# Performance work log

Measured on AMD Instinct MI355X. Metric: run time of the kernel, lower is better.

## Reference

```python
import jax, jax.numpy as jnp
import numpy as np

H, D = 4, 32  # num_heads, per-head out dim (out_feats=128)
N_AGENT, N_GT, N_UAV = 50000, 50000, 50000
E = 600000
IN = 64


def _gat(x_src, x_dst, src, dst, W_src, W_dst, al, ar, W_res, b, num_dst):
    """DGL-style bipartite GATConv with residual, bias and ReLU activation."""
    fs = (x_src @ W_src).reshape(-1, H, D)      # [Ns,H,D]
    fd = (x_dst @ W_dst).reshape(-1, H, D)      # [Nd,H,D]
    el = jnp.sum(fs * al, axis=-1)              # [Ns,H]
    er = jnp.sum(fd * ar, axis=-1)              # [Nd,H]
    e = jax.nn.leaky_relu(el[src] + er[dst], 0.2)          # [E,H]
    # segment softmax over incoming edges of each dst node
    emax = jax.ops.segment_max(e, dst, num_segments=num_dst)   # [Nd,H], -inf for deg-0
    ee = jnp.exp(e - emax[dst])
    denom = jax.ops.segment_sum(ee, dst, num_segments=num_dst)
    a = ee / denom[dst]                          # [E,H]
    msg = fs[src] * a[:, :, None]                # [E,H,D]
    rst = jax.ops.segment_sum(msg, dst, num_segments=num_dst)  # [Nd,H,D]; zeros for deg-0
    res = (x_dst @ W_res).reshape(-1, H, D)      # residual projection
    out = jax.nn.relu(rst + res + b.reshape(1, H, D))
    return out.reshape(num_dst, H * D)


def setup_inputs() -> dict:
    key = jax.random.key(0)
    ks = jax.random.split(key, 20)
    s = 0.1  # weight init scale
    return {
        'x_gt': jax.random.normal(ks[0], (N_GT, IN), jnp.float32),
        'x_uav': jax.random.normal(ks[1], (N_UAV, IN), jnp.float32),
        'x_agent': jax.random.normal(ks[2], (N_AGENT, IN), jnp.float32),
        'src_gt': jax.random.randint(ks[3], (E,), 0, N_GT, jnp.int32),
        'dst_gt': jax.random.randint(ks[4], (E,), 0, N_AGENT, jnp.int32),
        'src_uav': jax.random.randint(ks[5], (E,), 0, N_UAV, jnp.int32),
        'dst_uav': jax.random.randint(ks[6], (E,), 0, N_AGENT, jnp.int32),
        'W_src_gt': s * jax.random.normal(ks[7], (IN, H * D), jnp.float32),
        'W_dst_gt': s * jax.random.normal(ks[8], (IN, H * D), jnp.float32),
        'attn_l_gt': s * jax.random.normal(ks[9], (H, D), jnp.float32),
        'attn_r_gt': s * jax.random.normal(ks[10], (H, D), jnp.float32),
        'W_res_gt': s * jax.random.normal(ks[11], (IN, H * D), jnp.float32),
        'b_gt': jnp.zeros((H * D,), jnp.float32),
        'W_src_uav': s * jax.random.normal(ks[12], (IN, H * D), jnp.float32),
        'W_dst_uav': s * jax.random.normal(ks[13], (IN, H * D), jnp.float32),
        'attn_l_uav': s * jax.random.normal(ks[14], (H, D), jnp.float32),
        'attn_r_uav': s * jax.random.normal(ks[15], (H, D), jnp.float32),
        'W_res_uav': s * jax.random.normal(ks[16], (IN, H * D), jnp.float32),
        'b_uav': jnp.zeros((H * D,), jnp.float32),
        'W_f': s * jax.random.normal(ks[17], (2 * H * D, H * D), jnp.float32),
        'b_f': jnp.zeros((H * D,), jnp.float32),
    }


def reference(x_gt, x_uav, x_agent, src_gt, dst_gt, src_uav, dst_uav,
              W_src_gt, W_dst_gt, attn_l_gt, attn_r_gt, W_res_gt, b_gt,
              W_src_uav, W_dst_uav, attn_l_uav, attn_r_uav, W_res_uav, b_uav,
              W_f, b_f):
    h_gt = _gat(x_gt, x_agent, src_gt, dst_gt, W_src_gt, W_dst_gt,
                attn_l_gt, attn_r_gt, W_res_gt, b_gt, N_AGENT)
    h_uav = _gat(x_uav, x_agent, src_uav, dst_uav, W_src_uav, W_dst_uav,
                 attn_l_uav, attn_r_uav, W_res_uav, b_uav, N_AGENT)
    h = jnp.concatenate([h_gt, h_uav], axis=1)   # [N_agent, 256]
    return jax.nn.relu(h @ W_f + b_f)            # [N_agent, 128]
```

## Files before the change

### kernel.cpp

```cpp
#include <hip/hip_runtime.h>
#include <hip/hip_bf16.h>

using bf16 = __hip_bfloat16;

#define NA 50000
#define NE 600000

typedef __attribute__((ext_vector_type(8))) short short8;
typedef __attribute__((ext_vector_type(4))) float f32x4;

#define HBUF_B   0u
#define FS_B     25600000u
#define EL_B     51200000u
#define RECS_B   54400000u
#define CNT_B    73600000u
#define ROW_B    74000000u
#define TOPS_B   74400016u
#define FLAG_B   74400528u
#define WST_GT_B 74400544u
#define WST_UAV_B 74416928u
#define WRT_B    74433312u
#define WFT_B    74466080u
#define ELT_GT_B 74531616u
#define ELT_UAV_B 74533664u
#define ERT_B    74535712u
#define RANK_B   74537760u
#define WS_BYTES 79337760u

__device__ __forceinline__ float b2f(bf16 v) { return __bfloat162float(v); }

__device__ __forceinline__ float ldf(const void* p, size_t i, int f32) {
    return f32 ? ((const float*)p)[i] : b2f(((const bf16*)p)[i]);
}

__device__ __forceinline__ unsigned short f2bs(float v) {
    bf16 t = __float2bfloat16(v);
    return *(unsigned short*)&t;
}

__device__ __forceinline__ float lrelu_exp(float v) {
    v = v > 0.f ? v : 0.2f * v;
    return __expf(v);
}

__device__ __forceinline__ unsigned int pack_bf16x2(float a, float b) {
    return (unsigned int)f2bs(a) | ((unsigned int)f2bs(b) << 16);
}

__device__ __forceinline__ float lo_f(unsigned int u) { return __uint_as_float(u << 16); }
__device__ __forceinline__ float hi_f(unsigned int u) { return __uint_as_float(u & 0xffff0000u); }

__device__ __forceinline__ short8 ldfrag8(const void* p, size_t off, int f32) {
    if (!f32) return *(const short8*)((const unsigned short*)p + off);
    union { short8 s; unsigned int u[4]; } r;
    const float* fp = (const float*)p + off;
#pragma unroll
    for (int j = 0; j < 4; ++j) r.u[j] = pack_bf16x2(fp[2 * j], fp[2 * j + 1]);
    return r.s;
}

__device__ int probe_f32(const void* x0) {
    __shared__ int cnt;
    if (threadIdx.x == 0) cnt = 0;
    __syncthreads();
    const bf16* p = (const bf16*)x0;
    int bad = 0;
    for (int i = threadIdx.x; i < 1024; i += 256) {
        float av = fabsf(b2f(p[i]));
        if (!(av <= 1e6f)) bad++;
    }
    if (bad) atomicAdd(&cnt, bad);
    __syncthreads();
    return cnt > 8;
}

__global__ void HeteroVisionConv_29703993819529_kernel(
    const void* x0,
    const void* Wsg, const void* alg, const void* Wdg, const void* arg_,
    const void* Wsu, const void* alu, const void* Wdu, const void* aru,
    const void* Wrg, const void* Wru, const void* Wf,
    const int* dg, const int* du, unsigned int* cnt, unsigned int* rank,
    unsigned short* wsT_gt, unsigned short* wsT_uav, unsigned short* wrT,
    unsigned short* wfT, unsigned short* elT_gt, unsigned short* elT_uav,
    unsigned short* erT,
    int* flag, unsigned int* outp, long sent) {
    int b = blockIdx.x, t = threadIdx.x;
    if (b >= 21) {
        int idx = (b - 21) * 256 + t;
        if (idx >= 300000) return;
        int g = idx >= 150000;
        int e = (idx - g * 150000) * 4;
        int4 d4 = *(const int4*)((g ? du : dg) + e);
        unsigned int* c = cnt + g * NA;
        uint4 r4;
        r4.x = atomicAdd(&c[d4.x], 1u);
        r4.y = atomicAdd(&c[d4.y], 1u);
        r4.z = atomicAdd(&c[d4.z], 1u);
        r4.w = atomicAdd(&c[d4.w], 1u);
        *(uint4*)(rank + (size_t)g * NE + e) = r4;
        return;
    }
    int f32 = probe_f32(x0);
    if (b == 20) {
        if (t == 0) { flag[0] = f32; outp[sent] = 0x447A447Au; }
        return;
    }
    if (b < 8) {
        for (int i = t; i < 16 * 256; i += 256) {
            int n = b * 16 + (i >> 8), k = i & 255;
            wfT[n * 256 + k] = f2bs(ldf(Wf, (size_t)k * 128 + n, f32));
        }
    } else if (b < 12) {
        for (int i = t; i < 64 * 64; i += 256) {
            int n = (b - 8) * 64 + (i >> 6), k = i & 63;
            float v = (n < 128) ? ldf(Wrg, (size_t)k * 128 + n, f32)
                                : ldf(Wru, (size_t)k * 128 + (n - 128), f32);
            wrT[n * 64 + k] = f2bs(v);
        }
    } else if (b < 14) {
        for (int i = t; i < 64 * 64; i += 256) {
            int n = (b - 12) * 64 + (i >> 6), k = i & 63;
            wsT_gt[n * 64 + k] = f2bs(ldf(Wsg, (size_t)k * 128 + n, f32));
        }
    } else if (b < 16) {
        for (int i = t; i < 64 * 64; i += 256) {
            int n = (b - 14) * 64 + (i >> 6), k = i & 63;
            wsT_uav[n * 64 + k] = f2bs(ldf(Wsu, (size_t)k * 128 + n, f32));
        }
    } else {
        int m = b - 16;
        const void* Wm = (m == 0) ? Wsg : (m == 1) ? Wdg : (m == 2) ? Wsu : Wdu;
        const void* Am = (m == 0) ? alg : (m == 1) ? arg_ : (m == 2) ? alu : aru;
        int k = t >> 2, h = t & 3;
        float a = 0.f;
        for (int d = 0; d < 32; ++d)
            a += ldf(Wm, (size_t)k * 128 + h * 32 + d, f32) *
                 ldf(Am, (size_t)h * 32 + d, f32);
        unsigned short v = f2bs(a);
        if (m == 0) {
            elT_gt[h * 64 + k] = v;
            for (int i = t; i < 12 * 64; i += 256) elT_gt[(4 + (i >> 6)) * 64 + (i & 63)] = 0;
        } else if (m == 2) {
            elT_uav[h * 64 + k] = v;
            for (int i = t; i < 12 * 64; i += 256) elT_uav[(4 + (i >> 6)) * 64 + (i & 63)] = 0;
        } else if (m == 1) {
            erT[h * 64 + k] = v;
        } else {
            erT[(4 + h) * 64 + k] = v;
            for (int i = t; i < 8 * 64; i += 256) erT[(8 + (i >> 6)) * 64 + (i & 63)] = 0;
        }
    }
}

__global__ void node_fs_k(const void* xg, const void* xu,
                          const unsigned short* wsT_gt, const unsigned short* wsT_uav,
                          const unsigned short* elT_gt, const unsigned short* elT_uav,
                          float* elbase, bf16* fs, const int* flag) {
    int f32 = *flag;
    int bx = blockIdx.x, g = bx / 782, b = bx % 782;
    const void* A = g ? xu : xg;
    const unsigned short* WT = g ? wsT_uav : wsT_gt;
    const unsigned short* ET = g ? elT_uav : elT_gt;
    float* elout = elbase + (g ? 400000 : 0);
    bf16* out = fs + (size_t)g * NA * 128;
    __shared__ unsigned short Bt[128 * 72];
    int t = threadIdx.x;
    for (int i = t * 8; i < 128 * 64; i += 256 * 8) {
        short8 v = *(const short8*)(WT + i);
        int n = i >> 6, k = i & 63;
        *(short8*)&Bt[n * 72 + k] = v;
    }
    __syncthreads();
    int lane = t & 63, w = t >> 6;
    int m = lane & 15, quad = lane >> 4;
    int row = b * 64 + w * 16 + m;
    int rowc = row < NA ? row : NA - 1;
    short8 a0 = ldfrag8(A, (size_t)rowc * 64 + quad * 8, f32);
    short8 a1 = ldfrag8(A, (size_t)rowc * 64 + 32 + quad * 8, f32);
    f32x4 acc[8];
#pragma unroll
    for (int nt = 0; nt < 8; ++nt) acc[nt] = (f32x4){0.f, 0.f, 0.f, 0.f};
#pragma unroll
    for (int nt = 0; nt < 8; ++nt) {
        short8 b0 = *(const short8*)&Bt[(nt * 16 + m) * 72 + quad * 8];
        short8 b1 = *(const short8*)&Bt[(nt * 16 + m) * 72 + 32 + quad * 8];
        acc[nt] = __builtin_amdgcn_mfma_f32_16x16x32_bf16(a0, b0, acc[nt], 0, 0, 0);
        acc[nt] = __builtin_amdgcn_mfma_f32_16x16x32_bf16(a1, b1, acc[nt], 0, 0, 0);
    }
    f32x4 eacc = (f32x4){0.f, 0.f, 0.f, 0.f};
    {
        short8 e0 = *(const short8*)&ET[m * 64 + quad * 8];
        short8 e1 = *(const short8*)&ET[m * 64 + 32 + quad * 8];
        eacc = __builtin_amdgcn_mfma_f32_16x16x32_bf16(a0, e0, eacc, 0, 0, 0);
        eacc = __builtin_amdgcn_mfma_f32_16x16x32_bf16(a1, e1, eacc, 0, 0, 0);
    }
    int srow = b * 64 + w * 16 + quad * 4;
#pragma unroll
    for (int nt = 0; nt < 8; ++nt) {
#pragma unroll
        for (int r = 0; r < 4; ++r) {
            int rr = srow + r;
            if (rr < NA) out[(size_t)rr * 128 + nt * 16 + m] = __float2bfloat16(acc[nt][r]);
        }
    }
    if (m < 4) {
#pragma unroll
        for (int r = 0; r < 4; ++r) {
            int rr = srow + r;
            if (rr < NA) elout[(size_t)rr * 4 + m] = eacc[r];
        }
    }
}

__global__ void res_k(const void* xa, const unsigned short* wrT,
                      const unsigned short* erT,
                      const void* bg, const void* bu,
                      float* elbase, bf16* hbuf, const int* flag) {
    int f32 = *flag;
    int b = blockIdx.x;
    __shared__ unsigned short Bt[256 * 72];
    __shared__ float bl[256];
    int t = threadIdx.x;
    for (int i = t * 8; i < 256 * 64; i += 256 * 8) {
        short8 v = *(const short8*)(wrT + i);
        int n = i >> 6, k = i & 63;
        *(short8*)&Bt[n * 72 + k] = v;
    }
    bl[t] = (t < 128) ? ldf(bg, t, f32) : ldf(bu, t - 128, f32);
    __syncthreads();
    int lane = t & 63, w = t >> 6;
    int m = lane & 15, quad = lane >> 4;
    int row = b * 64 + w * 16 + m;
    int rowc = row < NA ? row : NA - 1;
    short8 a0 = ldfrag8(xa, (size_t)rowc * 64 + quad * 8, f32);
    short8 a1 = ldfrag8(xa, (size_t)rowc * 64 + 32 + quad * 8, f32);
    f32x4 acc[16];
#pragma unroll
    for (int nt = 0; nt < 16; ++nt) acc[nt] = (f32x4){0.f, 0.f, 0.f, 0.f};
#pragma unroll
    for (int nt = 0; nt < 16; ++nt) {
        short8 b0 = *(const short8*)&Bt[(nt * 16 + m) * 72 + quad * 8];
        short8 b1 = *(const short8*)&Bt[(nt * 16 + m) * 72 + 32 + quad * 8];
        acc[nt] = __builtin_amdgcn_mfma_f32_16x16x32_bf16(a0, b0, acc[nt], 0, 0, 0);
        acc[nt] = __builtin_amdgcn_mfma_f32_16x16x32_bf16(a1, b1, acc[nt], 0, 0, 0);
    }
    f32x4 eacc = (f32x4){0.f, 0.f, 0.f, 0.f};
    {
        short8 e0 = *(const short8*)&erT[m * 64 + quad * 8];
        short8 e1 = *(const short8*)&erT[m * 64 + 32 + quad * 8];
        eacc = __builtin_amdgcn_mfma_f32_16x16x32_bf16(a0, e0, eacc, 0, 0, 0);
        eacc = __builtin_amdgcn_mfma_f32_16x16x32_bf16(a1, e1, eacc, 0, 0, 0);
    }
    int srow = b * 64 + w * 16 + quad * 4;
#pragma unroll
    for (int nt = 0; nt < 16; ++nt) {
        int col = nt * 16 + m;
#pragma unroll
        for (int r = 0; r < 4; ++r) {
            int rr = srow + r;
            if (rr < NA)
                hbuf[(size_t)rr * 256 + col] = __float2bfloat16(acc[nt][r] + bl[col]);
        }
    }
    if (m < 8) {
        float* ero = (m < 4) ? (elbase + 200000) : (elbase + 600000);
        int mm = m & 3;
#pragma unroll
        for (int r = 0; r < 4; ++r) {
            int rr = srow + r;
            if (rr < NA) ero[(size_t)rr * 4 + mm] = eacc[r];
        }
    }
}

__global__ void scan1_k(const unsigned int* cnt, unsigned int* row, unsigned int* tops) {
    __shared__ unsigned int sh[256];
    int b = blockIdx.x, t = threadIdx.x;
    int base = b * 1024 + t * 4;
    unsigned int v[4];
    for (int j = 0; j < 4; ++j) v[j] = (base + j < 100000) ? cnt[base + j] : 0u;
    unsigned int s = v[0] + v[1] + v[2] + v[3];
    sh[t] = s;
    __syncthreads();
    for (int off = 1; off < 256; off <<= 1) {
        unsigned int x = (t >= off) ? sh[t - off] : 0u;
        __syncthreads();
        sh[t] += x;
        __syncthreads();
    }
    unsigned int run = sh[t] - s;
    for (int j = 0; j < 4; ++j) {
        if (base + j < 100000) row[base + j] = run;
        run += v[j];
    }
    if (t == 255) tops[b] = sh[255];
}

__global__ void scan2_k(unsigned int* tops, unsigned int* row) {
    __shared__ unsigned int sh[128];
    int t = threadIdx.x;
    unsigned int v = (t < 98) ? tops[t] : 0u;
    sh[t] = v;
    __syncthreads();
    for (int off = 1; off < 128; off <<= 1) {
        unsigned int x = (t >= off) ? sh[t - off] : 0u;
        __syncthreads();
        sh[t] += x;
        __syncthreads();
    }
    if (t < 98) tops[t] = sh[t] - v;
    if (t == 97) row[100000] = sh[97];
}

__global__ void scan3_k(unsigned int* row, const unsigned int* tops) {
    int b = blockIdx.x, t = threadIdx.x;
    unsigned int off = tops[b];
    for (int i = b * 1024 + t; i < b * 1024 + 1024; i += 256) {
        if (i < 100000) row[i] += off;
    }
}

__global__ void scatter_k(const int* sg, const int* dg, const int* su, const int* du,
                          const float* elbase, const unsigned int* row,
                          const unsigned int* rank, uint4* recs) {
    int idx = blockIdx.x * 256 + threadIdx.x;
    if (idx >= 2 * NE) return;
    int g = idx >= NE;
    int e = idx - g * NE;
    int s = (g ? su : sg)[e];
    int d = (g ? du : dg)[e];
    const float4* el4 = (const float4*)(elbase + (g ? 400000 : 0));
    const float4* er4 = (const float4*)(elbase + (g ? 600000 : 200000));
    unsigned int pos = row[g * NA + d] + rank[idx];
    float4 l = el4[s], r = er4[d];
    uint4 rec;
    rec.x = (unsigned int)s;
    rec.y = pack_bf16x2(lrelu_exp(l.x + r.x), lrelu_exp(l.y + r.y));
    rec.z = pack_bf16x2(lrelu_exp(l.z + r.z), lrelu_exp(l.w + r.w));
    rec.w = 0u;
    recs[pos] = rec;
}

__global__ void gather_k(const unsigned int* row, const uint4* recs,
                         const bf16* fs, bf16* hbuf) {
    int wid = (blockIdx.x * 256 + threadIdx.x) >> 6;
    int lane = threadIdx.x & 63;
    if (wid >= 2 * NA) return;
    int g = wid / NA, d = wid - g * NA;
    int eh = lane >> 5;
    int sl = lane & 31;
    int h = sl >> 3;
    int hsel = h >> 1, hodd = h & 1;
    unsigned int start = row[g * NA + d];
    unsigned int end   = row[g * NA + d + 1];
    const uint2* fsw2 = (const uint2*)(fs + (size_t)g * NA * 128);

    float denom = 0.f, a0 = 0.f, a1 = 0.f, a2 = 0.f, a3 = 0.f;
    unsigned int i = start;
    for (; i + 8 <= end; i += 8) {
        uint4 rr[4];
        uint2 uu[4];
#pragma unroll
        for (int j = 0; j < 4; ++j) rr[j] = recs[i + 2 * j + eh];
#pragma unroll
        for (int j = 0; j < 4; ++j) uu[j] = fsw2[(size_t)rr[j].x * 32 + sl];
#pragma unroll
        for (int j = 0; j < 4; ++j) {
            unsigned int pp = hsel ? rr[j].z : rr[j].y;
            float e = hodd ? hi_f(pp) : lo_f(pp);
            denom += e;
            a0 += lo_f(uu[j].x) * e;
            a1 += hi_f(uu[j].x) * e;
            a2 += lo_f(uu[j].y) * e;
            a3 += hi_f(uu[j].y) * e;
        }
    }
    for (; i + 2 <= end; i += 2) {
        uint4 rc = recs[i + eh];
        uint2 u = fsw2[(size_t)rc.x * 32 + sl];
        unsigned int pp = hsel ? rc.z : rc.y;
        float e = hodd ? hi_f(pp) : lo_f(pp);
        denom += e;
        a0 += lo_f(u.x) * e;
        a1 += hi_f(u.x) * e;
        a2 += lo_f(u.y) * e;
        a3 += hi_f(u.y) * e;
    }
    if (i < end) {
        uint4 rc = recs[i];
        uint2 u = fsw2[(size_t)rc.x * 32 + sl];
        unsigned int pp = hsel ? rc.z : rc.y;
        float e = hodd ? hi_f(pp) : lo_f(pp);
        if (eh) e = 0.f;
        denom += e;
        a0 += lo_f(u.x) * e;
        a1 += hi_f(u.x) * e;
        a2 += lo_f(u.y) * e;
        a3 += hi_f(u.y) * e;
    }
    denom += __shfl_xor(denom, 32, 64);
    a0 += __shfl_xor(a0, 32, 64);
    a1 += __shfl_xor(a1, 32, 64);
    a2 += __shfl_xor(a2, 32, 64);
    a3 += __shfl_xor(a3, 32, 64);
    if (eh == 0) {
        float inv = (end > start) ? 1.f / denom : 0.f;
        a0 *= inv; a1 *= inv; a2 *= inv; a3 *= inv;
        uint2* hp = (uint2*)(hbuf + (size_t)d * 256 + g * 128) + sl;
        uint2 rv = *hp;
        float v0 = a0 + lo_f(rv.x);
        float v1 = a1 + hi_f(rv.x);
        float v2 = a2 + lo_f(rv.y);
        float v3 = a3 + hi_f(rv.y);
        v0 = v0 > 0.f ? v0 : 0.f;
        v1 = v1 > 0.f ? v1 : 0.f;
        v2 = v2 > 0.f ? v2 : 0.f;
        v3 = v3 > 0.f ? v3 : 0.f;
        uint2 o;
        o.x = pack_bf16x2(v0, v1);
        o.y = pack_bf16x2(v2, v3);
        *hp = o;
    }
}

__global__ void final_k(const bf16* hbuf, const unsigned short* wfT,
                        const void* bfp, void* outp, const int* flag) {
    int f32 = *flag;
    int b = blockIdx.x;
    __shared__ unsigned short Bt[128 * 72];
    __shared__ float bl[128];
    int t = threadIdx.x;
    if (t < 128) bl[t] = ldf(bfp, t, f32);
    int lane = t & 63, w = t >> 6;
    int m = lane & 15, quad = lane >> 4;
    int row = b * 64 + w * 16 + m;
    int rowc = row < NA ? row : NA - 1;
    f32x4 acc[8];
#pragma unroll
    for (int nt = 0; nt < 8; ++nt) acc[nt] = (f32x4){0.f, 0.f, 0.f, 0.f};
    for (int kc = 0; kc < 4; ++kc) {
        __syncthreads();
        for (int i = t * 8; i < 128 * 64; i += 256 * 8) {
            int n = i >> 6, k = i & 63;
            short8 v = *(const short8*)(wfT + (size_t)n * 256 + kc * 64 + k);
            *(short8*)&Bt[n * 72 + k] = v;
        }
        __syncthreads();
        short8 a0 = *(const short8*)((const unsigned short*)hbuf +
                                     (size_t)rowc * 256 + kc * 64 + quad * 8);
        short8 a1 = *(const short8*)((const unsigned short*)hbuf +
                                     (size_t)rowc * 256 + kc * 64 + 32 + quad * 8);
#pragma unroll
        for (int nt = 0; nt < 8; ++nt) {
            short8 b0 = *(const short8*)&Bt[(nt * 16 + m) * 72 + quad * 8];
            short8 b1 = *(const short8*)&Bt[(nt * 16 + m) * 72 + 32 + quad * 8];
            acc[nt] = __builtin_amdgcn_mfma_f32_16x16x32_bf16(a0, b0, acc[nt], 0, 0, 0);
            acc[nt] = __builtin_amdgcn_mfma_f32_16x16x32_bf16(a1, b1, acc[nt], 0, 0, 0);
        }
    }
    int srow = b * 64 + w * 16 + quad * 4;
#pragma unroll
    for (int nt = 0; nt < 8; ++nt) {
        int col = nt * 16 + m;
        float bv = bl[col];
#pragma unroll
        for (int r = 0; r < 4; ++r) {
            int rr = srow + r;
            if (rr < NA) {
                float v = acc[nt][r] + bv;
                v = v > 0.f ? v : 0.f;
                if (f32) ((float*)outp)[(size_t)rr * 128 + col] = v;
                else ((bf16*)outp)[(size_t)rr * 128 + col] = __float2bfloat16(v);
            }
        }
    }
}

extern "C" void kernel_launch(void* const* d_in, const int* in_sizes, int n_in,
                              void* d_out, int out_size, void* d_ws, size_t ws_size,
                              hipStream_t stream) {
    const void* x_gt     = d_in[0];
    const void* x_uav    = d_in[1];
    const void* x_ag     = d_in[2];
    const int*  src_gt   = (const int*)d_in[3];
    const int*  dst_gt   = (const int*)d_in[4];
    const int*  src_uav  = (const int*)d_in[5];
    const int*  dst_uav  = (const int*)d_in[6];
    const void* Wsrc_gt  = d_in[7];
    const void* Wdst_gt  = d_in[8];
    const void* al_gt    = d_in[9];
    const void* ar_gt    = d_in[10];
    const void* Wres_gt  = d_in[11];
    const void* b_gt     = d_in[12];
    const void* Wsrc_uav = d_in[13];
    const void* Wdst_uav = d_in[14];
    const void* al_uav   = d_in[15];
    const void* ar_uav   = d_in[16];
    const void* Wres_uav = d_in[17];
    const void* b_uav    = d_in[18];
    const void* W_f      = d_in[19];
    const void* b_f      = d_in[20];

    char* wsb = (char*)d_ws;
    bf16* hbuf = (bf16*)(wsb + HBUF_B);
    bf16* fs = (bf16*)(wsb + FS_B);
    float* el = (float*)(wsb + EL_B);
    uint4* recs = (uint4*)(wsb + RECS_B);
    unsigned int* cnt = (unsigned int*)(wsb + CNT_B);
    unsigned int* row = (unsigned int*)(wsb + ROW_B);
    unsigned int* tops = (unsigned int*)(wsb + TOPS_B);
    int* flag = (int*)(wsb + FLAG_B);
    unsigned short* wsT_gt = (unsigned short*)(wsb + WST_GT_B);
    unsigned short* wsT_uav = (unsigned short*)(wsb + WST_UAV_B);
    unsigned short* wrT = (unsigned short*)(wsb + WRT_B);
    unsigned short* wfT = (unsigned short*)(wsb + WFT_B);
    unsigned short* elT_gt = (unsigned short*)(wsb + ELT_GT_B);
    unsigned short* elT_uav = (unsigned short*)(wsb + ELT_UAV_B);
    unsigned short* erT = (unsigned short*)(wsb + ERT_B);
    unsigned int* rank = (unsigned int*)(wsb + RANK_B);

    if (ws_size < (size_t)WS_BYTES) {
        hipMemsetAsync(d_out, 0x42, (size_t)out_size * 2, stream);
        return;
    }

    long sent = (long)out_size / 2 - 1;

    hipMemsetAsync(cnt, 0, 100000 * 4, stream);
    HeteroVisionConv_29703993819529_kernel<<<21 + 1172, 256, 0, stream>>>(
        x_gt, Wsrc_gt, al_gt, Wdst_gt, ar_gt, Wsrc_uav, al_uav, Wdst_uav, ar_uav,
        Wres_gt, Wres_uav, W_f, dst_gt, dst_uav, cnt, rank,
        wsT_gt, wsT_uav, wrT, wfT, elT_gt, elT_uav, erT,
        flag, (unsigned int*)d_out, sent);
    node_fs_k<<<1564, 256, 0, stream>>>(x_gt, x_uav, wsT_gt, wsT_uav,
                                        elT_gt, elT_uav, el, fs, flag);
    res_k<<<782, 256, 0, stream>>>(x_ag, wrT, erT, b_gt, b_uav, el, hbuf, flag);
    scan1_k<<<98, 256, 0, stream>>>(cnt, row, tops);
    scan2_k<<<1, 128, 0, stream>>>(tops, row);
    scan3_k<<<98, 256, 0, stream>>>(row, tops);
    scatter_k<<<4688, 256, 0, stream>>>(src_gt, dst_gt, src_uav, dst_uav,
                                        el, row, rank, recs);
    gather_k<<<25000, 256, 0, stream>>>(row, recs, fs, hbuf);
    final_k<<<782, 256, 0, stream>>>(hbuf, wfT, b_f, d_out, flag);
}
```

Measured before the change: 313.0 us.

## Widen gather to 16B loads, four edges per wave, prefetch next records

The gather kernel now splits each wave into four groups of 16 lanes, one edge per group, instead of two groups of 32. Each lane loads 16 bytes of the source feature row rather than 8. The edge records for the next 16 edges are software-prefetched while the current feature loads are consumed, and tail edges are masked rather than handled by separate cleanup loops. The aim is fewer, wider gather instructions and more memory-level parallelism per wave. The cost is more registers, an extra shuffle stage in the reduction, and wasted lanes on nodes with low in-degree.

```diff
diff --git a/kernel.cpp b/kernel.cpp
--- a/kernel.cpp
+++ b/kernel.cpp
@@ -347,78 +347,88 @@
     int lane = threadIdx.x & 63;
     if (wid >= 2 * NA) return;
     int g = wid / NA, d = wid - g * NA;
-    int eh = lane >> 5;
-    int sl = lane & 31;
-    int h = sl >> 3;
-    int hsel = h >> 1, hodd = h & 1;
+    int eg = lane >> 4;
+    int cl = lane & 15;
+    int hsel = cl >> 3;
+    int hodd = (cl >> 2) & 1;
     unsigned int start = row[g * NA + d];
     unsigned int end   = row[g * NA + d + 1];
-    const uint2* fsw2 = (const uint2*)(fs + (size_t)g * NA * 128);
-
-    float denom = 0.f, a0 = 0.f, a1 = 0.f, a2 = 0.f, a3 = 0.f;
-    unsigned int i = start;
-    for (; i + 8 <= end; i += 8) {
-        uint4 rr[4];
-        uint2 uu[4];
-#pragma unroll
-        for (int j = 0; j < 4; ++j) rr[j] = recs[i + 2 * j + eh];
-#pragma unroll
-        for (int j = 0; j < 4; ++j) uu[j] = fsw2[(size_t)rr[j].x * 32 + sl];
+    const uint4* fs4 = (const uint4*)(fs + (size_t)g * NA * 128);
+
+    float denom = 0.f;
+    float a[8];
+#pragma unroll
+    for (int k = 0; k < 8; ++k) a[k] = 0.f;
+
+    if (start < end) {
+        uint4 rr[4], rn[4];
 #pragma unroll
         for (int j = 0; j < 4; ++j) {
-            unsigned int pp = hsel ? rr[j].z : rr[j].y;
-            float e = hodd ? hi_f(pp) : lo_f(pp);
-            denom += e;
-            a0 += lo_f(uu[j].x) * e;
-            a1 += hi_f(uu[j].x) * e;
-            a2 += lo_f(uu[j].y) * e;
-            a3 += hi_f(uu[j].y) * e;
-        }
-    }
-    for (; i + 2 <= end; i += 2) {
-        uint4 rc = recs[i + eh];
-        uint2 u = fsw2[(size_t)rc.x * 32 + sl];
-        unsigned int pp = hsel ? rc.z : rc.y;
-        float e = hodd ? hi_f(pp) : lo_f(pp);
-        denom += e;
-        a0 += lo_f(u.x) * e;
-        a1 += hi_f(u.x) * e;
-        a2 += lo_f(u.y) * e;
-        a3 += hi_f(u.y) * e;
-    }
-    if (i < end) {
-        uint4 rc = recs[i];
-        uint2 u = fsw2[(size_t)rc.x * 32 + sl];
-        unsigned int pp = hsel ? rc.z : rc.y;
-        float e = hodd ? hi_f(pp) : lo_f(pp);
-        if (eh) e = 0.f;
-        denom += e;
-        a0 += lo_f(u.x) * e;
-        a1 += hi_f(u.x) * e;
-        a2 += lo_f(u.y) * e;
-        a3 += hi_f(u.y) * e;
-    }
+            unsigned int idx = start + 4 * j + eg;
+            rr[j] = recs[idx < end ? idx : end - 1];
+        }
+        for (unsigned int i = start; i < end; i += 16) {
+            uint4 uu[4];
+#pragma unroll
+            for (int j = 0; j < 4; ++j) uu[j] = fs4[(size_t)rr[j].x * 16 + cl];
+            unsigned int inext = i + 16;
+#pragma unroll
+            for (int j = 0; j < 4; ++j) {
+                unsigned int idx = inext + 4 * j + eg;
+                rn[j] = recs[idx < end ? idx : end - 1];
+            }
+#pragma unroll
+            for (int j = 0; j < 4; ++j) {
+                unsigned int idx = i + 4 * j + eg;
+                unsigned int pp = hsel ? rr[j].z : rr[j].y;
+                float e = hodd ? hi_f(pp) : lo_f(pp);
+                if (idx >= end) e = 0.f;
+                denom += e;
+                a[0] += lo_f(uu[j].x) * e;
+                a[1] += hi_f(uu[j].x) * e;
+                a[2] += lo_f(uu[j].y) * e;
+                a[3] += hi_f(uu[j].y) * e;
+                a[4] += lo_f(uu[j].z) * e;
+                a[5] += hi_f(uu[j].z) * e;
+                a[6] += lo_f(uu[j].w) * e;
+                a[7] += hi_f(uu[j].w) * e;
+            }
+#pragma unroll
+            for (int j = 0; j < 4; ++j) rr[j] = rn[j];
+        }
+    }
+#pragma unroll
+    for (int k = 0; k < 8; ++k) {
+        a[k] += __shfl_xor(a[k], 16, 64);
+        a[k] += __shfl_xor(a[k], 32, 64);
+    }
+    denom += __shfl_xor(denom, 16, 64);
     denom += __shfl_xor(denom, 32, 64);
-    a0 += __shfl_xor(a0, 32, 64);
-    a1 += __shfl_xor(a1, 32, 64);
-    a2 += __shfl_xor(a2, 32, 64);
-    a3 += __shfl_xor(a3, 32, 64);
-    if (eh == 0) {
+    if (lane < 16) {
         float inv = (end > start) ? 1.f / denom : 0.f;
-        a0 *= inv; a1 *= inv; a2 *= inv; a3 *= inv;
-        uint2* hp = (uint2*)(hbuf + (size_t)d * 256 + g * 128) + sl;
-        uint2 rv = *hp;
-        float v0 = a0 + lo_f(rv.x);
-        float v1 = a1 + hi_f(rv.x);
-        float v2 = a2 + lo_f(rv.y);
-        float v3 = a3 + hi_f(rv.y);
+        uint4* hp = (uint4*)(hbuf + (size_t)d * 256 + g * 128) + cl;
+        uint4 rv = *hp;
+        float v0 = a[0] * inv + lo_f(rv.x);
+        float v1 = a[1] * inv + hi_f(rv.x);
+        float v2 = a[2] * inv + lo_f(rv.y);
+        float v3 = a[3] * inv + hi_f(rv.y);
+        float v4 = a[4] * inv + lo_f(rv.z);
+        float v5 = a[5] * inv + hi_f(rv.z);
+        float v6 = a[6] * inv + lo_f(rv.w);
+        float v7 = a[7] * inv + hi_f(rv.w);
         v0 = v0 > 0.f ? v0 : 0.f;
         v1 = v1 > 0.f ? v1 : 0.f;
         v2 = v2 > 0.f ? v2 : 0.f;
         v3 = v3 > 0.f ? v3 : 0.f;
-        uint2 o;
+        v4 = v4 > 0.f ? v4 : 0.f;
+        v5 = v5 > 0.f ? v5 : 0.f;
+        v6 = v6 > 0.f ? v6 : 0.f;
+        v7 = v7 > 0.f ? v7 : 0.f;
+        uint4 o;
         o.x = pack_bf16x2(v0, v1);
         o.y = pack_bf16x2(v2, v3);
+        o.z = pack_bf16x2(v4, v5);
+        o.w = pack_bf16x2(v6, v7);
         *hp = o;
     }
 }
```

Result: faster. 303.0 us (-3.2%).
